# Kernel tuning notes

Hardware: AMD Instinct MI355X
Metric: run time of the kernel (lower is better)

## Reference

```python
import jax, jax.numpy as jnp
import numpy as np

N_E = 1024
E_DIM = 256
BETA = 0.25


def setup_inputs() -> dict:
    key = jax.random.key(0)
    k1, k2 = jax.random.split(key)
    z = jax.random.normal(k1, (32, E_DIM, 2048), dtype=jnp.float32)  # [B, e_dim, T]
    # nn.Embedding weight init: uniform(-1/n_e, 1/n_e)
    embedding = jax.random.uniform(k2, (N_E, E_DIM), dtype=jnp.float32,
                                   minval=-1.0 / N_E, maxval=1.0 / N_E)
    return {"z": z, "embedding": embedding}


def reference(z, embedding):
    # z: [B, e_dim, T] -> [B, T, e_dim]
    zt = jnp.transpose(z, (0, 2, 1))
    B, T, C = zt.shape
    zf = zt.reshape(-1, C)  # [N, e_dim]
    n_e = embedding.shape[0]
    # squared L2 distances via ||a||^2 + ||b||^2 - 2 a.b  -> [N, n_e]
    d = (jnp.sum(zf * zf, axis=1, keepdims=True)
         + jnp.sum(embedding * embedding, axis=1)
         - 2.0 * jnp.matmul(zf, embedding.T))
    idx = jnp.argmin(d, axis=1)  # [N]
    # one-hot @ embedding == direct gather
    z_q = embedding[idx].reshape(B, T, C)
    loss = (BETA * jnp.mean((jax.lax.stop_gradient(z_q) - zt) ** 2)
            + jnp.mean((z_q - jax.lax.stop_gradient(zt)) ** 2))
    # straight-through estimator
    z_q_st = zt + jax.lax.stop_gradient(z_q - zt)
    # e_mean = mean of one-hot encodings == normalized code usage counts
    counts = jnp.zeros((n_e,), dtype=zf.dtype).at[idx].add(1.0)
    e_mean = counts / idx.shape[0]
    perplexity = jnp.exp(-jnp.sum(e_mean * jnp.log(e_mean + 1e-10)))
    z_q_out = jnp.transpose(z_q_st, (0, 2, 1))  # back to [B, e_dim, T]
    return (z_q_out, loss, perplexity, idx)
```

## Files before the change

kernel.cpp:

```cpp
#include <hip/hip_runtime.h>

#define B_ 32
#define C_ 256
#define T_ 2048
#define N_ 65536
#define NE_ 1024
#define NELEM 16777216
#define TAU 1.75e-4f
#define WLCAP 8192
#define RPB 8

typedef _Float16 half8 __attribute__((ext_vector_type(8)));
typedef float f32x4 __attribute__((ext_vector_type(4)));


__global__ void k_prep(const float* __restrict__ emb, half8* __restrict__ ebuf,
                       float* __restrict__ enorm, float* __restrict__ et) {
  int code = blockIdx.x * blockDim.x + threadIdx.x;
  const float4* row = reinterpret_cast<const float4*>(emb + (size_t)code * C_);
  double sum = 0.0;
#pragma unroll
  for (int k = 0; k < C_ / 4; ++k) {
    float4 v = row[k];
    sum = fma((double)v.x, (double)v.x, sum);
    sum = fma((double)v.y, (double)v.y, sum);
    sum = fma((double)v.z, (double)v.z, sum);
    sum = fma((double)v.w, (double)v.w, sum);
    et[(k * 4 + 0) * NE_ + code] = v.x;
    et[(k * 4 + 1) * NE_ + code] = v.y;
    et[(k * 4 + 2) * NE_ + code] = v.z;
    et[(k * 4 + 3) * NE_ + code] = v.w;
  }
  enorm[code] = (float)sum;
  const int ct = code >> 4, c = code & 15;
#pragma unroll
  for (int s = 0; s < 8; ++s) {
#pragma unroll
    for (int g = 0; g < 4; ++g) {
      float4 v0 = row[s * 8 + g * 2];
      float4 v1 = row[s * 8 + g * 2 + 1];
      half8 hv;
      hv[0] = (_Float16)v0.x; hv[1] = (_Float16)v0.y;
      hv[2] = (_Float16)v0.z; hv[3] = (_Float16)v0.w;
      hv[4] = (_Float16)v1.x; hv[5] = (_Float16)v1.y;
      hv[6] = (_Float16)v1.z; hv[7] = (_Float16)v1.w;
      ebuf[(ct * 8 + s) * 64 + g * 16 + c] = hv;
    }
  }
}

__device__ __forceinline__ void stage_tile(const half8* __restrict__ ebuf,
                                           half8* bsbase, int ctp, int w, int l) {
#pragma unroll
  for (int j = 0; j < 4; ++j) {
    const half8* gp = ebuf + (size_t)ctp * 1024 + (w * 4 + j) * 64 + l;
    half8* lp = bsbase + (w * 4 + j) * 64;
    __builtin_amdgcn_global_load_lds(
        (const __attribute__((address_space(1))) unsigned int*)gp,
        (__attribute__((address_space(3))) unsigned int*)lp, 16, 0, 0);
  }
}

__launch_bounds__(256, 2)
__global__ void k_vq(const float* __restrict__ z, const half8* __restrict__ ebuf,
                     const float* __restrict__ enorm, int* __restrict__ idx_i,
                     float* __restrict__ idx_f, int* __restrict__ counts,
                     int* __restrict__ nflag, int* __restrict__ worklist,
                     float* __restrict__ sse) {
  __shared__ half8 Bs[2][1024];
  const int tid = threadIdx.x;
  const int w = tid >> 6;
  const int l = tid & 63;
  const int col = l & 15;
  const int g = l >> 4;
  const int n0 = blockIdx.x * 128;
  const int b = n0 >> 11;
  const int t0 = (n0 & (T_ - 1)) + w * 32;
  const float* zc0 = z + (size_t)b * C_ * T_ + t0 + col;
  const float* zc1 = zc0 + 16;

  stage_tile(ebuf, &Bs[0][0], 0, w, l);

  half8 A0[8], A1[8];
  float s0 = 0.f, s1 = 0.f;
#pragma unroll
  for (int s = 0; s < 8; ++s) {
    half8 h0, h1;
#pragma unroll
    for (int i = 0; i < 8; ++i) {
      const size_t ko = (size_t)(32 * s + 8 * g + i) * T_;
      float zf0 = zc0[ko], zf1 = zc1[ko];
      h0[i] = (_Float16)zf0;
      h1[i] = (_Float16)zf1;
      s0 = fmaf(zf0, zf0, s0);
      s1 = fmaf(zf1, zf1, s1);
    }
    A0[s] = h0; A1[s] = h1;
  }
  s0 += __shfl_xor(s0, 16); s0 += __shfl_xor(s0, 32);
  s1 += __shfl_xor(s1, 16); s1 += __shfl_xor(s1, 32);

  float b1s[2][4], b2s[2][4]; int b1i[2][4];
#pragma unroll
  for (int rt = 0; rt < 2; ++rt)
#pragma unroll
    for (int q = 0; q < 4; ++q) { b1s[rt][q] = 3.4e38f; b2s[rt][q] = 3.4e38f; b1i[rt][q] = 0; }

  const f32x4 zero4 = {0.f, 0.f, 0.f, 0.f};
  __syncthreads();

  int cur = 0;
  for (int ctp = 0; ctp < 32; ++ctp) {
    if (ctp < 31) stage_tile(ebuf, &Bs[cur ^ 1][0], ctp + 1, w, l);
    const half8* bp = &Bs[cur][l];
    f32x4 a00 = zero4, a01 = zero4, a10 = zero4, a11 = zero4;
#pragma unroll
    for (int s = 0; s < 8; ++s) {
      half8 bf = bp[s * 64];
      a00 = __builtin_amdgcn_mfma_f32_16x16x32_f16(A0[s], bf, a00, 0, 0, 0);
      a10 = __builtin_amdgcn_mfma_f32_16x16x32_f16(A1[s], bf, a10, 0, 0, 0);
    }
#pragma unroll
    for (int s = 0; s < 8; ++s) {
      half8 bf = bp[(8 + s) * 64];
      a01 = __builtin_amdgcn_mfma_f32_16x16x32_f16(A0[s], bf, a01, 0, 0, 0);
      a11 = __builtin_amdgcn_mfma_f32_16x16x32_f16(A1[s], bf, a11, 0, 0, 0);
    }
    const float en0 = enorm[ctp * 32 + col];
    const float en1 = enorm[ctp * 32 + 16 + col];
    const int cb0 = ctp * 32 + col, cb1 = ctp * 32 + 16 + col;
#pragma unroll
    for (int q = 0; q < 4; ++q) {
      {
        float sc = fmaf(-2.f, a00[q], en0);
        float nb2 = fminf(b2s[0][q], fmaxf(b1s[0][q], sc));
        bool lt = sc < b1s[0][q];
        b2s[0][q] = nb2; b1i[0][q] = lt ? cb0 : b1i[0][q]; b1s[0][q] = fminf(b1s[0][q], sc);
      }
      {
        float sc = fmaf(-2.f, a10[q], en0);
        float nb2 = fminf(b2s[1][q], fmaxf(b1s[1][q], sc));
        bool lt = sc < b1s[1][q];
        b2s[1][q] = nb2; b1i[1][q] = lt ? cb0 : b1i[1][q]; b1s[1][q] = fminf(b1s[1][q], sc);
      }
      {
        float sc = fmaf(-2.f, a01[q], en1);
        float nb2 = fminf(b2s[0][q], fmaxf(b1s[0][q], sc));
        bool lt = sc < b1s[0][q];
        b2s[0][q] = nb2; b1i[0][q] = lt ? cb1 : b1i[0][q]; b1s[0][q] = fminf(b1s[0][q], sc);
      }
      {
        float sc = fmaf(-2.f, a11[q], en1);
        float nb2 = fminf(b2s[1][q], fmaxf(b1s[1][q], sc));
        bool lt = sc < b1s[1][q];
        b2s[1][q] = nb2; b1i[1][q] = lt ? cb1 : b1i[1][q]; b1s[1][q] = fminf(b1s[1][q], sc);
      }
    }
    __syncthreads();
    cur ^= 1;
  }

#pragma unroll
  for (int m = 1; m < 16; m <<= 1) {
#pragma unroll
    for (int rt = 0; rt < 2; ++rt)
#pragma unroll
      for (int q = 0; q < 4; ++q) {
        float o1 = __shfl_xor(b1s[rt][q], m);
        int oi = __shfl_xor(b1i[rt][q], m);
        float o2 = __shfl_xor(b2s[rt][q], m);
        float hi = fmaxf(b1s[rt][q], o1);
        b2s[rt][q] = fminf(fminf(b2s[rt][q], o2), hi);
        if (o1 < b1s[rt][q] || (o1 == b1s[rt][q] && oi < b1i[rt][q])) {
          b1s[rt][q] = o1; b1i[rt][q] = oi;
        }
      }
  }
  float rsum[2][4];
#pragma unroll
  for (int q = 0; q < 4; ++q) {
    rsum[0][q] = __shfl(s0, g * 4 + q);
    rsum[1][q] = __shfl(s1, g * 4 + q);
  }
  if (col == 0) {
    float local = 0.f;
#pragma unroll
    for (int rt = 0; rt < 2; ++rt)
#pragma unroll
      for (int q = 0; q < 4; ++q) {
        int n = n0 + w * 32 + rt * 16 + g * 4 + q;
        idx_i[n] = b1i[rt][q];
        idx_f[n] = (float)b1i[rt][q];
        atomicAdd(&counts[b1i[rt][q]], 1);
        if (b2s[rt][q] - b1s[rt][q] < TAU) {
          int p = atomicAdd(nflag, 1);
          if (p < WLCAP) worklist[p] = n;
        } else {
          local += rsum[rt][q] + b1s[rt][q];
        }
      }
    atomicAdd(sse, local);
  }
}

__global__ void k_zstage(const float* __restrict__ z, const int* __restrict__ nflag,
                         const int* __restrict__ worklist, float* __restrict__ zstage,
                         float* __restrict__ szfbuf) {
  __shared__ double wred[4];
  const int tid = threadIdx.x;
  int cnt = nflag[0];
  if (cnt > WLCAP) cnt = WLCAP;
  for (int wi = blockIdx.x; wi < cnt; wi += gridDim.x) {
    int n = worklist[wi];
    int b = n >> 11, t = n & (T_ - 1);
    float zv = z[(size_t)b * C_ * T_ + (size_t)tid * T_ + t];
    zstage[(size_t)wi * C_ + tid] = zv;
    double p = (double)zv * (double)zv;
#pragma unroll
    for (int m = 32; m > 0; m >>= 1) p += __shfl_down(p, m);
    if ((tid & 63) == 0) wred[tid >> 6] = p;
    __syncthreads();
    if (tid == 0)
      szfbuf[wi] = (float)(wred[0] + wred[1] + wred[2] + wred[3]);
    __syncthreads();
  }
}

__global__ void k_repair(const float* __restrict__ zstage, const float* __restrict__ szfbuf,
                         const float* __restrict__ et, const float* __restrict__ enorm,
                         const int* __restrict__ nflag, const int* __restrict__ worklist,
                         unsigned long long* __restrict__ keys) {
  __shared__ float zs[RPB][C_];
  __shared__ unsigned long long kred[RPB][256];
  const int tid = threadIdx.x;
  int cnt = nflag[0];
  if (cnt > WLCAP) cnt = WLCAP;
  const int ngroups = (cnt + RPB - 1) / RPB;
  const int nunits = ngroups * 4;
  for (int u = blockIdx.x; u < nunits; u += gridDim.x) {
    const int grp = u >> 2;
    const int quarter = u & 3;
    const int base = grp * RPB;
#pragma unroll
    for (int r = 0; r < RPB; ++r) {
      int wi = base + r; if (wi >= cnt) wi = cnt - 1;
      zs[r][tid] = zstage[(size_t)wi * C_ + tid];
    }
    __syncthreads();
    const int j = quarter * 256 + tid;
    float acc[RPB];
#pragma unroll
    for (int r = 0; r < RPB; ++r) acc[r] = 0.f;
#pragma unroll 4
    for (int k4 = 0; k4 < C_ / 4; ++k4) {
      float e0 = et[(k4 * 4 + 0) * NE_ + j];
      float e1 = et[(k4 * 4 + 1) * NE_ + j];
      float e2 = et[(k4 * 4 + 2) * NE_ + j];
      float e3 = et[(k4 * 4 + 3) * NE_ + j];
#pragma unroll
      for (int r = 0; r < RPB; ++r) {
        acc[r] = fmaf(zs[r][k4 * 4 + 0], e0, acc[r]);
        acc[r] = fmaf(zs[r][k4 * 4 + 1], e1, acc[r]);
        acc[r] = fmaf(zs[r][k4 * 4 + 2], e2, acc[r]);
        acc[r] = fmaf(zs[r][k4 * 4 + 3], e3, acc[r]);
      }
    }
    const float en = enorm[j];
#pragma unroll
    for (int r = 0; r < RPB; ++r) {
      int wi = base + r; if (wi >= cnt) wi = cnt - 1;
      float X = szfbuf[wi] + en;
      float Y = 2.0f * acc[r];
      float d = X - Y;
      unsigned int du = __float_as_uint(d);
      unsigned int sortable = (du & 0x80000000u) ? ~du : (du | 0x80000000u);
      kred[r][tid] = ((unsigned long long)sortable << 32) | (unsigned int)j;
    }
    __syncthreads();
    for (int o = 128; o > 0; o >>= 1) {
      if (tid < o) {
#pragma unroll
        for (int r = 0; r < RPB; ++r) {
          unsigned long long ok = kred[r][tid + o];
          if (ok < kred[r][tid]) kred[r][tid] = ok;
        }
      }
      __syncthreads();
    }
    if (tid < RPB && base + tid < cnt)
      atomicMin(&keys[base + tid], kred[tid][0]);
    __syncthreads();
  }
}

__global__ void k_fix(const int* __restrict__ nflag, const int* __restrict__ worklist,
                      const unsigned long long* __restrict__ keys,
                      int* __restrict__ idx_i, float* __restrict__ idx_f,
                      int* __restrict__ counts, float* __restrict__ sse) {
  int cnt = nflag[0];
  if (cnt > WLCAP) cnt = WLCAP;
  int wi = blockIdx.x * blockDim.x + threadIdx.x;
  if (wi < cnt) {
    int n = worklist[wi];
    unsigned long long key = keys[wi];
    int nw = (int)(key & 0xFFFFFFFFull);
    unsigned int s = (unsigned int)(key >> 32);
    unsigned int du = (s & 0x80000000u) ? (s & 0x7FFFFFFFu) : ~s;
    atomicAdd(sse, __uint_as_float(du));
    int old = idx_i[n];
    if (nw != old) {
      idx_i[n] = nw; idx_f[n] = (float)nw;
      atomicAdd(&counts[old], -1);
      atomicAdd(&counts[nw], 1);
    }
  }
}

__launch_bounds__(256, 4)
__global__ void k_gather(const float* __restrict__ emb, const int* __restrict__ idxv,
                         float* __restrict__ zq) {
  __shared__ int ids[32];
  __shared__ float tile[32 * 260];
  const int tid = threadIdx.x;
  const int blk = blockIdx.x;
  const int b = blk >> 6;
  const int t0 = (blk & 63) << 5;
  const int n0 = (b << 11) + t0;
  if (tid < 32) ids[tid] = idxv[n0 + tid];
  __syncthreads();
  const int r = tid & 31;
  const int q = tid >> 5;
  {
    const float4* er = reinterpret_cast<const float4*>(emb) + ((size_t)ids[r] << 6) + (q << 3);
    float4* dst = reinterpret_cast<float4*>(&tile[r * 260 + (q << 5)]);
#pragma unroll
    for (int j = 0; j < 8; ++j) dst[j] = er[j];
  }
  __syncthreads();
  const size_t base = (((size_t)b << 8) << 11) + t0;
#pragma unroll 8
  for (int it = 0; it < 32; ++it) {
    const int c = (it << 3) + q;
    zq[base + ((size_t)c << 11) + r] = tile[r * 260 + c];
  }
}

__global__ void k_final(const int* __restrict__ counts, const float* __restrict__ sse,
                        float* __restrict__ out_loss, float* __restrict__ out_perp) {
  __shared__ float red[256];
  int tid = threadIdx.x;
  float s = 0.f;
  for (int j = tid; j < NE_; j += 256) {
    float em = (float)counts[j] * (1.0f / (float)N_);
    s += em * logf(em + 1e-10f);
  }
  red[tid] = s;
  __syncthreads();
  for (int o = 128; o > 0; o >>= 1) {
    if (tid < o) red[tid] += red[tid + o];
    __syncthreads();
  }
  if (tid == 0) {
    out_perp[0] = expf(-red[0]);
    out_loss[0] = (0.25f + 1.0f) * sse[0] / (float)NELEM;
  }
}

extern "C" void kernel_launch(void* const* d_in, const int* in_sizes, int n_in,
                              void* d_out, int out_size, void* d_ws, size_t ws_size,
                              hipStream_t stream) {
  const float* z = (const float*)d_in[0];
  const float* emb = (const float*)d_in[1];
  float* out = (float*)d_out;
  float* zq_out = out;
  float* out_loss = out + NELEM;
  float* out_perp = out + NELEM + 1;
  float* out_idx = out + NELEM + 2;

  int* ws_counts = (int*)d_ws;
  float* ws_enorm = (float*)d_ws + 1024;
  float* ws_sse = (float*)d_ws + 2048;
  int* ws_nflag = (int*)d_ws + 2049;
  unsigned long long* ws_keys = (unsigned long long*)((float*)d_ws + 2056);
  int* ws_idx = (int*)d_ws + 18440;
  int* ws_worklist = (int*)d_ws + 83976;
  float* ws_szf = (float*)d_ws + 92168;
  half8* ws_ebuf = (half8*)((float*)d_ws + 100360);
  float* ws_et = (float*)d_ws + 231432;
  float* ws_zstage = (float*)d_ws + 493576;

  hipMemsetAsync(d_ws, 0, 8224, stream);
  hipMemsetAsync((char*)d_ws + 8224, 0xFF, WLCAP * 8, stream);

  k_prep<<<NE_ / 64, 64, 0, stream>>>(emb, ws_ebuf, ws_enorm, ws_et);
  k_vq<<<N_ / 128, 256, 0, stream>>>(z, ws_ebuf, ws_enorm, ws_idx, out_idx,
                                     ws_counts, ws_nflag, ws_worklist, ws_sse);
  k_zstage<<<2048, 256, 0, stream>>>(z, ws_nflag, ws_worklist, ws_zstage, ws_szf);
  k_repair<<<2048, 256, 0, stream>>>(ws_zstage, ws_szf, ws_et, ws_enorm,
                                     ws_nflag, ws_worklist, ws_keys);
  k_fix<<<WLCAP / 256, 256, 0, stream>>>(ws_nflag, ws_worklist, ws_keys,
                                         ws_idx, out_idx, ws_counts, ws_sse);
  k_gather<<<2048, 256, 0, stream>>>(emb, ws_idx, zq_out);
  k_final<<<1, 256, 0, stream>>>(ws_counts, ws_sse, out_loss, out_perp);
}
```

Before: 185.4 us.

## Load codebook fragments directly from global into registers, dropping LDS staging

Replaces the double-buffered LDS staging of the fp16 codebook (global_load_lds plus a __syncthreads per tile) with per-wave register prefetch of B fragments straight from global memory, issued between the MFMA halves. This removes LDS traffic and block-wide barriers. In exchange each wave loads the whole codebook itself through L1/L2, four times the global traffic per block, and holds 16 extra half8 registers, which may strain the 2-blocks-per-CU occupancy target.

```diff
diff --git a/kernel.cpp b/kernel.cpp
--- a/kernel.cpp
+++ b/kernel.cpp
@@ -49,25 +49,12 @@
   }
 }
 
-__device__ __forceinline__ void stage_tile(const half8* __restrict__ ebuf,
-                                           half8* bsbase, int ctp, int w, int l) {
-#pragma unroll
-  for (int j = 0; j < 4; ++j) {
-    const half8* gp = ebuf + (size_t)ctp * 1024 + (w * 4 + j) * 64 + l;
-    half8* lp = bsbase + (w * 4 + j) * 64;
-    __builtin_amdgcn_global_load_lds(
-        (const __attribute__((address_space(1))) unsigned int*)gp,
-        (__attribute__((address_space(3))) unsigned int*)lp, 16, 0, 0);
-  }
-}
-
 __launch_bounds__(256, 2)
 __global__ void k_vq(const float* __restrict__ z, const half8* __restrict__ ebuf,
                      const float* __restrict__ enorm, int* __restrict__ idx_i,
                      float* __restrict__ idx_f, int* __restrict__ counts,
                      int* __restrict__ nflag, int* __restrict__ worklist,
                      float* __restrict__ sse) {
-  __shared__ half8 Bs[2][1024];
   const int tid = threadIdx.x;
   const int w = tid >> 6;
   const int l = tid & 63;
@@ -79,8 +66,6 @@
   const float* zc0 = z + (size_t)b * C_ * T_ + t0 + col;
   const float* zc1 = zc0 + 16;
 
-  stage_tile(ebuf, &Bs[0][0], 0, w, l);
-
   half8 A0[8], A1[8];
   float s0 = 0.f, s1 = 0.f;
 #pragma unroll
@@ -106,58 +91,66 @@
 #pragma unroll
     for (int q = 0; q < 4; ++q) { b1s[rt][q] = 3.4e38f; b2s[rt][q] = 3.4e38f; b1i[rt][q] = 0; }
 
-  const f32x4 zero4 = {0.f, 0.f, 0.f, 0.f};
-  __syncthreads();
-
-  int cur = 0;
-  for (int ctp = 0; ctp < 32; ++ctp) {
-    if (ctp < 31) stage_tile(ebuf, &Bs[cur ^ 1][0], ctp + 1, w, l);
-    const half8* bp = &Bs[cur][l];
-    f32x4 a00 = zero4, a01 = zero4, a10 = zero4, a11 = zero4;
-#pragma unroll
-    for (int s = 0; s < 8; ++s) {
-      half8 bf = bp[s * 64];
-      a00 = __builtin_amdgcn_mfma_f32_16x16x32_f16(A0[s], bf, a00, 0, 0, 0);
-      a10 = __builtin_amdgcn_mfma_f32_16x16x32_f16(A1[s], bf, a10, 0, 0, 0);
-    }
-#pragma unroll
-    for (int s = 0; s < 8; ++s) {
-      half8 bf = bp[(8 + s) * 64];
-      a01 = __builtin_amdgcn_mfma_f32_16x16x32_f16(A0[s], bf, a01, 0, 0, 0);
-      a11 = __builtin_amdgcn_mfma_f32_16x16x32_f16(A1[s], bf, a11, 0, 0, 0);
-    }
-    const float en0 = enorm[ctp * 32 + col];
-    const float en1 = enorm[ctp * 32 + 16 + col];
-    const int cb0 = ctp * 32 + col, cb1 = ctp * 32 + 16 + col;
+  auto fold = [&](const f32x4& c00, const f32x4& c10, const f32x4& c01, const f32x4& c11,
+                  float en0, float en1, int cb0, int cb1) {
 #pragma unroll
     for (int q = 0; q < 4; ++q) {
       {
-        float sc = fmaf(-2.f, a00[q], en0);
+        float sc = fmaf(-2.f, c00[q], en0);
         float nb2 = fminf(b2s[0][q], fmaxf(b1s[0][q], sc));
         bool lt = sc < b1s[0][q];
         b2s[0][q] = nb2; b1i[0][q] = lt ? cb0 : b1i[0][q]; b1s[0][q] = fminf(b1s[0][q], sc);
       }
       {
-        float sc = fmaf(-2.f, a10[q], en0);
+        float sc = fmaf(-2.f, c10[q], en0);
         float nb2 = fminf(b2s[1][q], fmaxf(b1s[1][q], sc));
         bool lt = sc < b1s[1][q];
         b2s[1][q] = nb2; b1i[1][q] = lt ? cb0 : b1i[1][q]; b1s[1][q] = fminf(b1s[1][q], sc);
       }
       {
-        float sc = fmaf(-2.f, a01[q], en1);
+        float sc = fmaf(-2.f, c01[q], en1);
         float nb2 = fminf(b2s[0][q], fmaxf(b1s[0][q], sc));
         bool lt = sc < b1s[0][q];
         b2s[0][q] = nb2; b1i[0][q] = lt ? cb1 : b1i[0][q]; b1s[0][q] = fminf(b1s[0][q], sc);
       }
       {
-        float sc = fmaf(-2.f, a11[q], en1);
+        float sc = fmaf(-2.f, c11[q], en1);
         float nb2 = fminf(b2s[1][q], fmaxf(b1s[1][q], sc));
         bool lt = sc < b1s[1][q];
         b2s[1][q] = nb2; b1i[1][q] = lt ? cb1 : b1i[1][q]; b1s[1][q] = fminf(b1s[1][q], sc);
       }
     }
-    __syncthreads();
-    cur ^= 1;
+  };
+
+  const half8* bp = ebuf + l;
+  half8 Bf0[8], Bf1[8];
+#pragma unroll
+  for (int s = 0; s < 8; ++s) { Bf0[s] = bp[s * 64]; Bf1[s] = bp[(8 + s) * 64]; }
+  const f32x4 zero4 = {0.f, 0.f, 0.f, 0.f};
+
+  for (int ctp = 0; ctp < 32; ++ctp) {
+    f32x4 a00 = zero4, a01 = zero4, a10 = zero4, a11 = zero4;
+#pragma unroll
+    for (int s = 0; s < 8; ++s) {
+      a00 = __builtin_amdgcn_mfma_f32_16x16x32_f16(A0[s], Bf0[s], a00, 0, 0, 0);
+      a10 = __builtin_amdgcn_mfma_f32_16x16x32_f16(A1[s], Bf0[s], a10, 0, 0, 0);
+    }
+    if (ctp < 31) {
+#pragma unroll
+      for (int s = 0; s < 8; ++s) Bf0[s] = bp[((ctp + 1) * 16 + s) * 64];
+    }
+#pragma unroll
+    for (int s = 0; s < 8; ++s) {
+      a01 = __builtin_amdgcn_mfma_f32_16x16x32_f16(A0[s], Bf1[s], a01, 0, 0, 0);
+      a11 = __builtin_amdgcn_mfma_f32_16x16x32_f16(A1[s], Bf1[s], a11, 0, 0, 0);
+    }
+    if (ctp < 31) {
+#pragma unroll
+      for (int s = 0; s < 8; ++s) Bf1[s] = bp[((ctp + 1) * 16 + 8 + s) * 64];
+    }
+    const float en0 = enorm[ctp * 32 + col];
+    const float en1 = enorm[ctp * 32 + 16 + col];
+    fold(a00, a10, a01, a11, en0, en1, ctp * 32 + col, ctp * 32 + 16 + col);
   }
 
 #pragma unroll
```

After: 184.2 us. About the same (-0.7%).
